# Optimization experiments

Measured on AMD Instinct MI355X. Metric: run time of the kernel, lower is better.

Reference implementation:

```python
import jax, jax.numpy as jnp
import numpy as np

B = 128
VOCAB = 32000
EMB = 256
HID = 1024  # units*2 with units=512


def gru_step(x, h, Wi, Wr, bi, br):
    # Keras GRU, reset_after=True, gate order [z, r, h]
    gi = x @ Wi + bi          # [B, 3H]
    gr = h @ Wr + br          # [B, 3H]
    iz, ir, ih = jnp.split(gi, 3, axis=-1)
    rz, rr, rh = jnp.split(gr, 3, axis=-1)
    z = jax.nn.sigmoid(iz + rz)
    r = jax.nn.sigmoid(ir + rr)
    hh = jnp.tanh(ih + r * rh)
    return z * h + (1.0 - z) * hh


def setup_inputs() -> dict:
    key = jax.random.key(0)
    ks = jax.random.split(key, 16)
    s = 0.02
    inp = {
        "x": jax.random.randint(ks[0], (B, 1), 0, VOCAB),
        "h0": jax.random.normal(ks[1], (B, HID), jnp.float32),
        "h1": jax.random.normal(ks[2], (B, HID), jnp.float32),
        "emb": jax.random.normal(ks[3], (VOCAB, EMB), jnp.float32) * s,
        "Wi0": jax.random.normal(ks[4], (EMB, 3 * HID), jnp.float32) * s,
        "Wr0": jax.random.normal(ks[5], (HID, 3 * HID), jnp.float32) * s,
        "bi0": jnp.zeros((3 * HID,), jnp.float32),
        "br0": jnp.zeros((3 * HID,), jnp.float32),
        "Wi1": jax.random.normal(ks[6], (HID, 3 * HID), jnp.float32) * s,
        "Wr1": jax.random.normal(ks[7], (HID, 3 * HID), jnp.float32) * s,
        "bi1": jnp.zeros((3 * HID,), jnp.float32),
        "br1": jnp.zeros((3 * HID,), jnp.float32),
        "ffW": jax.random.normal(ks[8], (HID, VOCAB), jnp.float32) * s,
        "ffb": jnp.zeros((VOCAB,), jnp.float32),
    }
    return inp


def reference(x, h0, h1, emb, Wi0, Wr0, bi0, br0, Wi1, Wr1, bi1, br1, ffW, ffb):
    e = emb[x[:, 0]]                       # [B, EMB] (seq_len == 1)
    h0n = gru_step(e, h0, Wi0, Wr0, bi0, br0)   # [B, H]
    h1n = gru_step(h0n, h1, Wi1, Wr1, bi1, br1)  # [B, H]
    logits = h1n @ ffW + ffb               # [B, VOCAB]
    return logits, h0n, h1n
```

## Files before the change

kernel.cpp:

```cpp
#include <hip/hip_runtime.h>

#define HIDN 1024
#define G3 3072
#define NVOCAB 32000

typedef __bf16 bf16x8 __attribute__((ext_vector_type(8)));
typedef float f32x4 __attribute__((ext_vector_type(4)));
typedef unsigned short ushort4v __attribute__((ext_vector_type(4)));

__device__ __forceinline__ unsigned short f2bf(float f) {
  union { float f; unsigned int u; } v; v.f = f;
  unsigned int u = v.u;
  return (unsigned short)((u + 0x7fffu + ((u >> 16) & 1u)) >> 16);
}

__device__ __forceinline__ float sigmoidf_(float x) {
  return 1.0f / (1.0f + __expf(-x));
}

__device__ __forceinline__ void gload16(const void* g, void* l) {
  __builtin_amdgcn_global_load_lds(
      (const __attribute__((address_space(1))) unsigned int*)g,
      (__attribute__((address_space(3))) unsigned int*)l, 16, 0, 0);
}

template <bool AF32, bool GATHER>
__device__ __forceinline__ void gemm32(
    const void* __restrict__ Aptr, int lda, const int* __restrict__ rix,
    int k0, int Kh, const float* __restrict__ W, int ldw, int n0,
    const float* __restrict__ bias, float* __restrict__ C, int ldc,
    char* smem) {
  constexpr int ABYTES = AF32 ? 16384 : 8192;
  constexpr int SBUF = 4096 + ABYTES;
  constexpr int NA = AF32 ? 4 : 2;
  const int t = threadIdx.x;
  const int w = t >> 6, lane = t & 63;
  const int l15 = lane & 15, kg = lane >> 4;
  const int rh = w >> 1, ct = w & 1;

  f32x4 acc[4];
#pragma unroll
  for (int r = 0; r < 4; ++r) acc[r] = (f32x4)0.0f;

  const size_t srcB = (size_t)(w * 8 + (lane >> 3)) * ldw + n0 +
                      ((lane & 7) ^ ((w & 1) << 2)) * 4;
  size_t srcA[NA];
  if constexpr (AF32) {
#pragma unroll
    for (int m = 0; m < NA; ++m) {
      int row = (w * 4 + m) * 8 + (lane >> 3);
      size_t rb;
      if constexpr (GATHER)
        rb = (size_t)rix[row] * lda;
      else
        rb = (size_t)row * lda;
      srcA[m] = rb + (((lane & 7) ^ (row & 7)) << 2);
    }
  } else {
#pragma unroll
    for (int m = 0; m < NA; ++m) {
      int g = (w * 2 + m) * 64 + lane;
      int row = g >> 2, uq = g & 3;
      srcA[m] = (size_t)row * lda + ((uq ^ ((row >> 1) & 3)) << 3);
    }
  }

  auto stage = [&](int c, int sel) {
    char* bb = smem + sel * SBUF;
    char* ab = bb + 4096;
    const int kbase = k0 + c * 32;
    gload16(W + (size_t)kbase * ldw + srcB, bb + w * 1024);
    if constexpr (AF32) {
#pragma unroll
      for (int m = 0; m < NA; ++m)
        gload16((const float*)Aptr + srcA[m] + kbase, ab + (w * 4 + m) * 1024);
    } else {
#pragma unroll
      for (int m = 0; m < NA; ++m)
        gload16((const unsigned short*)Aptr + srcA[m] + kbase,
                ab + (w * 2 + m) * 1024);
    }
  };

  const int NC = Kh >> 5;
  stage(0, 0);
  stage(1, 1);

  const int cl = ct * 16 + l15;
  for (int c = 0; c < NC; ++c) {
    if (c + 1 < NC) {
      if constexpr (AF32)
        asm volatile("s_waitcnt vmcnt(5)" ::: "memory");
      else
        asm volatile("s_waitcnt vmcnt(3)" ::: "memory");
    } else {
      asm volatile("s_waitcnt vmcnt(0)" ::: "memory");
    }
    __builtin_amdgcn_s_barrier();
    asm volatile("" ::: "memory");

    if (c + 2 < NC) stage(c + 2, (c + 2) % 3);

    const int sel = c % 3;
    const float* bbf = (const float*)(smem + sel * SBUF);
    const char* abf = smem + sel * SBUF + 4096;

    bf16x8 bfr;
#pragma unroll
    for (int j = 0; j < 8; ++j) {
      int r = kg * 8 + j;
      int q = (cl >> 2) ^ (((r >> 3) & 1) << 2);
      bfr[j] = (__bf16)bbf[r * 32 + q * 4 + (cl & 3)];
    }
#pragma unroll
    for (int rt = 0; rt < 4; ++rt) {
      const int row = rh * 64 + rt * 16 + l15;
      bf16x8 af;
      if constexpr (AF32) {
        const float* ar = (const float*)abf + row * 32;
        float4 fa = *(const float4*)(ar + (((kg * 2 + 0) ^ (l15 & 7)) << 2));
        float4 fb = *(const float4*)(ar + (((kg * 2 + 1) ^ (l15 & 7)) << 2));
        af[0] = (__bf16)fa.x; af[1] = (__bf16)fa.y;
        af[2] = (__bf16)fa.z; af[3] = (__bf16)fa.w;
        af[4] = (__bf16)fb.x; af[5] = (__bf16)fb.y;
        af[6] = (__bf16)fb.z; af[7] = (__bf16)fb.w;
      } else {
        af = *(const bf16x8*)((const unsigned short*)abf + row * 32 +
                              ((kg ^ ((row >> 1) & 3)) << 3));
      }
      acc[rt] =
          __builtin_amdgcn_mfma_f32_16x16x32_bf16(af, bfr, acc[rt], 0, 0, 0);
    }
  }

  const int col = n0 + cl;
  const float bs = bias ? bias[col] : 0.0f;
#pragma unroll
  for (int rt = 0; rt < 4; ++rt) {
    const int rb = rh * 64 + rt * 16 + kg * 4;
#pragma unroll
    for (int j = 0; j < 4; ++j)
      C[(size_t)(rb + j) * ldc + col] = acc[rt][j] + bs;
  }
}

template <bool XF32>
__global__ __launch_bounds__(256) void gru_gemms_kernel(
    const void* __restrict__ X, int KX, const int* __restrict__ xidx,
    const float* __restrict__ H, const float* __restrict__ Wi,
    const float* __restrict__ bi, const float* __restrict__ Wr,
    const float* __restrict__ br, float* __restrict__ giP,
    float* __restrict__ grP) {
  __shared__ char smem[3 * 20480];
  const int bid = blockIdx.x;
  const int mat = bid / 192, rem = bid % 192;
  const int ks = rem / 96, cb = rem % 96;
  if (mat == 0) {
    const int Kh = KX >> 1;
    gemm32<XF32, XF32>(X, KX, xidx, ks * Kh, Kh, Wi, G3, cb * 32,
                       ks ? nullptr : bi, giP + (size_t)ks * 128 * G3, G3,
                       smem);
  } else {
    gemm32<true, false>(H, HIDN, nullptr, ks * 512, 512, Wr, G3, cb * 32,
                        ks ? nullptr : br, grP + (size_t)ks * 128 * G3, G3,
                        smem);
  }
}

__global__ __launch_bounds__(256) void gates_kernel(
    const float* __restrict__ giP, const float* __restrict__ grP,
    const float* __restrict__ hfp, float* __restrict__ hout,
    ushort4v* __restrict__ hbf) {
  int i4 = blockIdx.x * 256 + threadIdx.x;
  int b = i4 >> 8, n = (i4 & 255) * 4;
  const float* g0 = giP + (size_t)b * G3;
  const float* g1 = g0 + (size_t)128 * G3;
  const float* r0 = grP + (size_t)b * G3;
  const float* r1 = r0 + (size_t)128 * G3;
  float4 izv = *(const float4*)(g0 + n);
  float4 izw = *(const float4*)(g1 + n);
  float4 rzv = *(const float4*)(r0 + n);
  float4 rzw = *(const float4*)(r1 + n);
  float4 irv = *(const float4*)(g0 + 1024 + n);
  float4 irw = *(const float4*)(g1 + 1024 + n);
  float4 rrv = *(const float4*)(r0 + 1024 + n);
  float4 rrw = *(const float4*)(r1 + 1024 + n);
  float4 ihv = *(const float4*)(g0 + 2048 + n);
  float4 ihw = *(const float4*)(g1 + 2048 + n);
  float4 rhv = *(const float4*)(r0 + 2048 + n);
  float4 rhw = *(const float4*)(r1 + 2048 + n);
  float4 hv = *(const float4*)(hfp + (size_t)b * HIDN + n);
  float4 ov;
  ushort4v obf;
#pragma unroll
  for (int j = 0; j < 4; ++j) {
    float iz = (&izv.x)[j] + (&izw.x)[j], rz = (&rzv.x)[j] + (&rzw.x)[j];
    float ir = (&irv.x)[j] + (&irw.x)[j], rr = (&rrv.x)[j] + (&rrw.x)[j];
    float ih = (&ihv.x)[j] + (&ihw.x)[j], rh = (&rhv.x)[j] + (&rhw.x)[j];
    float z = sigmoidf_(iz + rz);
    float r = sigmoidf_(ir + rr);
    float hh = tanhf(ih + r * rh);
    float h = (&hv.x)[j];
    float o = z * h + (1.0f - z) * hh;
    (&ov.x)[j] = o;
    obf[j] = f2bf(o);
  }
  *(float4*)(hout + (size_t)b * HIDN + n) = ov;
  hbf[i4] = obf;
}

__global__ __launch_bounds__(256) void ff_kernel(
    const unsigned short* __restrict__ A, const float* __restrict__ W,
    const float* __restrict__ bias, float* __restrict__ C) {
  __shared__ char smem[49152];
  const int n0 = blockIdx.x * 64;
  const int t = threadIdx.x;
  const int w = t >> 6, lane = t & 63;
  const int l15 = lane & 15, kg = lane >> 4;

  f32x4 acc[8];
#pragma unroll
  for (int r = 0; r < 8; ++r) acc[r] = (f32x4)0.0f;

  size_t srcB[2], srcA[2];
#pragma unroll
  for (int m = 0; m < 2; ++m) {
    int g = (w * 2 + m) * 64 + lane;
    {
      int r = g >> 4, q = g & 15;
      int p = q ^ (((r >> 3) & 1) << 2);
      srcB[m] = (size_t)r * NVOCAB + n0 + p * 4;
    }
    {
      int row = g >> 2, uq = g & 3;
      int up = uq ^ ((row >> 1) & 3);
      srcA[m] = (size_t)row * HIDN + up * 8;
    }
  }

  auto stage = [&](int c, int sel) {
    char* bb = smem + sel * 8192;
    char* ab = smem + 24576 + sel * 8192;
    int kbase = c * 32;
#pragma unroll
    for (int m = 0; m < 2; ++m)
      gload16(W + (size_t)kbase * NVOCAB + srcB[m], bb + (w * 2 + m) * 1024);
#pragma unroll
    for (int m = 0; m < 2; ++m)
      gload16(A + srcA[m] + kbase, ab + (w * 2 + m) * 1024);
  };

  stage(0, 0);
  stage(1, 1);

  const int NC = HIDN >> 5;
  const int cl = w * 16 + l15;
  for (int c = 0; c < NC; ++c) {
    if (c + 1 < NC)
      asm volatile("s_waitcnt vmcnt(4)" ::: "memory");
    else
      asm volatile("s_waitcnt vmcnt(0)" ::: "memory");
    __builtin_amdgcn_s_barrier();
    asm volatile("" ::: "memory");

    if (c + 2 < NC) stage(c + 2, (c + 2) % 3);

    int sel = c % 3;
    const float* bbf = (const float*)(smem + sel * 8192);
    const unsigned short* abf =
        (const unsigned short*)(smem + 24576 + sel * 8192);

    bf16x8 bfr;
#pragma unroll
    for (int j = 0; j < 8; ++j) {
      int r = kg * 8 + j;
      int q = (cl >> 2) ^ (((r >> 3) & 1) << 2);
      bfr[j] = (__bf16)bbf[r * 64 + q * 4 + (cl & 3)];
    }
#pragma unroll
    for (int rt = 0; rt < 8; ++rt) {
      int row = rt * 16 + l15;
      bf16x8 af =
          *(const bf16x8*)(abf + row * 32 + ((kg ^ ((row >> 1) & 3)) << 3));
      acc[rt] =
          __builtin_amdgcn_mfma_f32_16x16x32_bf16(af, bfr, acc[rt], 0, 0, 0);
    }
  }

  const int col = n0 + cl;
  const float bs = bias[col];
#pragma unroll
  for (int rt = 0; rt < 8; ++rt) {
    int rb = rt * 16 + kg * 4;
#pragma unroll
    for (int j = 0; j < 4; ++j)
      C[(size_t)(rb + j) * NVOCAB + col] = acc[rt][j] + bs;
  }
}

extern "C" void kernel_launch(void* const* d_in, const int* in_sizes, int n_in,
                              void* d_out, int out_size, void* d_ws,
                              size_t ws_size, hipStream_t stream) {
  const int* x = (const int*)d_in[0];
  const float* h0 = (const float*)d_in[1];
  const float* h1 = (const float*)d_in[2];
  const float* emb = (const float*)d_in[3];
  const float* Wi0 = (const float*)d_in[4];
  const float* Wr0 = (const float*)d_in[5];
  const float* bi0 = (const float*)d_in[6];
  const float* br0 = (const float*)d_in[7];
  const float* Wi1 = (const float*)d_in[8];
  const float* Wr1 = (const float*)d_in[9];
  const float* bi1 = (const float*)d_in[10];
  const float* br1 = (const float*)d_in[11];
  const float* ffW = (const float*)d_in[12];
  const float* ffb = (const float*)d_in[13];

  float* out = (float*)d_out;
  float* logits = out;
  float* h0n = out + 4096000;
  float* h1n = out + 4227072;

  float* giP = (float*)d_ws;
  float* grP = giP + 2 * 128 * G3;
  unsigned short* h0nb = (unsigned short*)(grP + 2 * 128 * G3);
  unsigned short* h1nb = h0nb + 131072;

  gru_gemms_kernel<true><<<384, 256, 0, stream>>>(emb, 256, x, h0, Wi0, bi0,
                                                  Wr0, br0, giP, grP);
  gates_kernel<<<128, 256, 0, stream>>>(giP, grP, h0, h0n, (ushort4v*)h0nb);

  gru_gemms_kernel<false><<<384, 256, 0, stream>>>(h0nb, 1024, nullptr, h1,
                                                   Wi1, bi1, Wr1, br1, giP,
                                                   grP);
  gates_kernel<<<128, 256, 0, stream>>>(giP, grP, h1, h1n, (ushort4v*)h1nb);

  ff_kernel<<<500, 256, 0, stream>>>(h1nb, ffW, ffb, logits);
}
```

Baseline: 56.89 us.

## Stage FF weights through registers as transposed bf16 in LDS

The fp32 weight tile is no longer copied straight from global memory into LDS. Each thread now loads 8 strided fp32 values into registers, converts them to bf16 and writes one swizzled 16-byte vector into LDS, double-buffered across iterations. This lets the MFMA B fragment be fetched with a single vector LDS read instead of eight scalar reads and conversions, and it shrinks the LDS footprint. In exchange, the global loads become 4-byte per-thread loads rather than 16-byte direct-to-LDS loads, register pressure rises, and the wait counts must track a different number of outstanding loads.

Result: slower. 66.66 us (+17.2%).

```diff
diff --git a/kernel.cpp b/kernel.cpp
--- a/kernel.cpp
+++ b/kernel.cpp
@@ -212,7 +212,8 @@
 __global__ __launch_bounds__(256) void ff_kernel(
     const unsigned short* __restrict__ A, const float* __restrict__ W,
     const float* __restrict__ bias, float* __restrict__ C) {
-  __shared__ char smem[49152];
+  constexpr int SBUF = 12288;
+  __shared__ char smem[3 * SBUF];
   const int n0 = blockIdx.x * 64;
   const int t = threadIdx.x;
   const int w = t >> 6, lane = t & 63;
@@ -222,61 +223,68 @@
 #pragma unroll
   for (int r = 0; r < 8; ++r) acc[r] = (f32x4)0.0f;
 
-  size_t srcB[2], srcA[2];
+  size_t srcA[2];
 #pragma unroll
   for (int m = 0; m < 2; ++m) {
     int g = (w * 2 + m) * 64 + lane;
-    {
-      int r = g >> 4, q = g & 15;
-      int p = q ^ (((r >> 3) & 1) << 2);
-      srcB[m] = (size_t)r * NVOCAB + n0 + p * 4;
-    }
-    {
-      int row = g >> 2, uq = g & 3;
-      int up = uq ^ ((row >> 1) & 3);
-      srcA[m] = (size_t)row * HIDN + up * 8;
-    }
-  }
-
-  auto stage = [&](int c, int sel) {
-    char* bb = smem + sel * 8192;
-    char* ab = smem + 24576 + sel * 8192;
-    int kbase = c * 32;
+    int row = g >> 2, uq = g & 3;
+    srcA[m] = (size_t)row * HIDN + ((uq ^ ((row >> 1) & 3)) << 3);
+  }
+  auto stageA = [&](int c, int sel) {
+    char* ab = smem + sel * SBUF;
 #pragma unroll
     for (int m = 0; m < 2; ++m)
-      gload16(W + (size_t)kbase * NVOCAB + srcB[m], bb + (w * 2 + m) * 1024);
-#pragma unroll
-    for (int m = 0; m < 2; ++m)
-      gload16(A + srcA[m] + kbase, ab + (w * 2 + m) * 1024);
+      gload16(A + srcA[m] + c * 32, ab + (w * 2 + m) * 1024);
   };
 
-  stage(0, 0);
-  stage(1, 1);
+  const int bc = t & 63, bu = t >> 6;
+  const float* Wbase = W + (size_t)bu * 8 * NVOCAB + n0 + bc;
+  const int bwoff = bc * 32 + ((bu ^ ((bc >> 1) & 3)) << 3);
+  const int cl = w * 16 + l15;
+  const int brdoff = cl * 32 + ((kg ^ ((cl >> 1) & 3)) << 3);
+
+  float bv0[8], bv1[8];
+  auto loadB = [&](int c, float* r8) {
+    const float* p = Wbase + (size_t)c * 32 * NVOCAB;
+#pragma unroll
+    for (int j = 0; j < 8; ++j) r8[j] = p[(size_t)j * NVOCAB];
+  };
+  auto writeB = [&](const float* r8, int sel) {
+    bf16x8 v;
+#pragma unroll
+    for (int j = 0; j < 8; ++j) v[j] = (__bf16)r8[j];
+    *(bf16x8*)((unsigned short*)(smem + sel * SBUF + 8192) + bwoff) = v;
+  };
 
   const int NC = HIDN >> 5;
-  const int cl = w * 16 + l15;
+  loadB(0, bv0);
+  stageA(0, 0);
+  loadB(1, bv1);
+  stageA(1, 1);
+  __builtin_amdgcn_sched_barrier(0);
+  writeB(bv0, 0);
+
   for (int c = 0; c < NC; ++c) {
     if (c + 1 < NC)
-      asm volatile("s_waitcnt vmcnt(4)" ::: "memory");
+      asm volatile("s_waitcnt vmcnt(10) lgkmcnt(0)" ::: "memory");
     else
-      asm volatile("s_waitcnt vmcnt(0)" ::: "memory");
+      asm volatile("s_waitcnt vmcnt(0) lgkmcnt(0)" ::: "memory");
     __builtin_amdgcn_s_barrier();
     asm volatile("" ::: "memory");
 
-    if (c + 2 < NC) stage(c + 2, (c + 2) % 3);
-
-    int sel = c % 3;
-    const float* bbf = (const float*)(smem + sel * 8192);
-    const unsigned short* abf =
-        (const unsigned short*)(smem + 24576 + sel * 8192);
-
-    bf16x8 bfr;
-#pragma unroll
-    for (int j = 0; j < 8; ++j) {
-      int r = kg * 8 + j;
-      int q = (cl >> 2) ^ (((r >> 3) & 1) << 2);
-      bfr[j] = (__bf16)bbf[r * 64 + q * 4 + (cl & 3)];
-    }
+    float* bnext = (c & 1) ? bv1 : bv0;
+    if (c + 2 < NC) {
+      loadB(c + 2, bnext);
+      stageA(c + 2, (c + 2) % 3);
+      __builtin_amdgcn_sched_barrier(0);
+    }
+
+    const int sel = c % 3;
+    const unsigned short* abf = (const unsigned short*)(smem + sel * SBUF);
+    const unsigned short* btf =
+        (const unsigned short*)(smem + sel * SBUF + 8192);
+
+    bf16x8 bfr = *(const bf16x8*)(btf + brdoff);
 #pragma unroll
     for (int rt = 0; rt < 8; ++rt) {
       int row = rt * 16 + l15;
@@ -285,6 +293,8 @@
       acc[rt] =
           __builtin_amdgcn_mfma_f32_16x16x32_bf16(af, bfr, acc[rt], 0, 0, 0);
     }
+
+    if (c + 1 < NC) writeB((c & 1) ? bv0 : bv1, (c + 1) % 3);
   }
 
   const int col = n0 + cl;
```
